# Kernel tuning notes

Hardware: AMD Instinct MI355X
Metric: run time of the kernel (lower is better)

Reference implementation:

```python
import jax, jax.numpy as jnp
import numpy as np

B = 65536   # batch
F = 256     # FeatureDim
E = 8       # experts_num
D = 64      # ExpertOutDim
EPS = 1e-5  # BatchNorm eps (eval mode: running stats)


def _bn(x, g, be, m, v):
    # BatchNorm1d in eval mode
    return (x - m) * jax.lax.rsqrt(v + EPS) * g + be


def setup_inputs() -> dict:
    key = jax.random.key(0)
    ks = jax.random.split(key, 40)
    r = lambda i, s: jax.random.normal(ks[i], s, dtype=jnp.float32) * 0.05
    u = lambda i, s: jax.random.uniform(ks[i], s, dtype=jnp.float32)
    return dict(
        signal_em=jax.random.normal(ks[0], (B, F), dtype=jnp.float32),
        muti_em=jax.random.normal(ks[1], (B, F), dtype=jnp.float32),
        similarity=jax.random.uniform(ks[2], (B,), dtype=jnp.float32),
        w=u(3, ()), b=u(4, ()),
        ps_W=r(5, (F, 256)), ps_b=r(6, (256,)), ps_g=u(7, (256,)), ps_be=r(8, (256,)), ps_m=r(9, (256,)), ps_v=u(10, (256,)) + 0.5,
        pm_W=r(11, (F, 256)), pm_b=r(12, (256,)), pm_g=u(13, (256,)), pm_be=r(14, (256,)), pm_m=r(15, (256,)), pm_v=u(16, (256,)) + 0.5,
        c1_W=r(17, (2 * F, 64)), c1_b=r(18, (64,)), c1_g=u(19, (64,)), c1_be=r(20, (64,)), c1_m=r(21, (64,)), c1_v=u(22, (64,)) + 0.5,
        c2_W=r(23, (64, 64)), c2_b=r(24, (64,)), c2_g=u(25, (64,)), c2_be=r(26, (64,)), c2_m=r(27, (64,)), c2_v=u(28, (64,)) + 0.5,
        c3_W=r(29, (64, 2)), c3_b=r(30, (2,)),
        e_W1=r(31, (E, 2 * F, 256)), e_b1=r(32, (E, 256)),
        e_W2=r(33, (E, 256, D)), e_b2=r(34, (E, D)),
        s_W1=r(35, (E, E)), s_b1=r(36, (E,)), s_W2=r(37, (E, E)), s_b2=r(38, (E,)),
    )


def reference(signal_em, muti_em, similarity, w, b,
              ps_W, ps_b, ps_g, ps_be, ps_m, ps_v,
              pm_W, pm_b, pm_g, pm_be, pm_m, pm_v,
              c1_W, c1_b, c1_g, c1_be, c1_m, c1_v,
              c2_W, c2_b, c2_g, c2_be, c2_m, c2_v,
              c3_W, c3_b,
              e_W1, e_b1, e_W2, e_b2,
              s_W1, s_b1, s_W2, s_b2):
    sim_weight = similarity[:, None] * w + b                        # [B,1]
    sig = jax.nn.relu(_bn(signal_em @ ps_W + ps_b, ps_g, ps_be, ps_m, ps_v))
    sig = sim_weight * sig
    mut = jax.nn.relu(_bn(muti_em @ pm_W + pm_b, pm_g, pm_be, pm_m, pm_v))
    temp = jnp.concatenate([sig, mut], axis=1)                      # [B, 512]

    # classifier head (dropout = identity in eval mode)
    h = jax.nn.relu(_bn(temp @ c1_W + c1_b, c1_g, c1_be, c1_m, c1_v))
    h = jax.nn.relu(_bn(h @ c2_W + c2_b, c2_g, c2_be, c2_m, c2_v))
    pre_score = h @ c3_W + c3_b                                     # [B,2]

    # all E experts as one batched GEMM (Expert_net has dropout p=0)
    eh = jax.nn.relu(jnp.einsum('bf,efh->beh', temp, e_W1) + e_b1)  # [B,E,256]
    eo = jax.nn.relu(jnp.einsum('beh,ehd->bed', eh, e_W2) + e_b2)   # [B,E,64]

    # SE-style gating: avg/max pool over expert-out dim (kernel==D -> scalar)
    att_ave = eo.mean(axis=-1)                                      # [B,E]
    att_max = eo.max(axis=-1)                                       # [B,E]
    senet = lambda x: jax.nn.gelu(x @ s_W1 + s_b1, approximate=False) @ s_W2 + s_b2
    wts = jax.nn.sigmoid(senet(att_ave) + senet(att_max))           # [B,E]

    gate_out = jnp.einsum('bed,be->bd', eo, wts)                    # [B,D]
    return (gate_out, pre_score)
```

## Files before the change

### kernel.cpp

```cpp
#include <hip/hip_runtime.h>
#include <math.h>

using u32 = unsigned int;
using u16 = unsigned short;
typedef __attribute__((ext_vector_type(4))) float f4;
typedef __attribute__((ext_vector_type(4))) u32 u4;
typedef __attribute__((ext_vector_type(2))) u32 u2;
typedef __attribute__((ext_vector_type(8))) __bf16 b8;

union U4B8 { u4 u; b8 b; };

__device__ __forceinline__ u16 f2b(float x) {
  u32 u = __float_as_uint(x);
  u32 r = (u + 0x7FFFu + ((u >> 16) & 1u)) >> 16;
  return (u16)r;
}
__device__ __forceinline__ u32 pack2(float a, float b) { return (u32)f2b(a) | ((u32)f2b(b) << 16); }
__device__ __forceinline__ f4 mfma16(b8 a, b8 b, f4 c) {
  return __builtin_amdgcn_mfma_f32_16x16x32_bf16(a, b, c, 0, 0, 0);
}

#define FENCE() asm volatile("" ::: "memory")
#define RAWBAR() do { FENCE(); __builtin_amdgcn_s_barrier(); FENCE(); __builtin_amdgcn_sched_barrier(0); } while (0)
#define VMW(nlit) do { asm volatile("s_waitcnt vmcnt(" nlit ")" ::: "memory"); __builtin_amdgcn_sched_barrier(0); } while (0)
#define LGKM0() do { asm volatile("s_waitcnt lgkmcnt(0)" ::: "memory"); __builtin_amdgcn_sched_barrier(0); } while (0)
#define LBAR() do { LGKM0(); __builtin_amdgcn_s_barrier(); FENCE(); __builtin_amdgcn_sched_barrier(0); } while (0)

template <int NB>
__device__ __forceinline__ void gstage(const u16* g, u16* l, int t) {
#pragma unroll
  for (int i = 0; i < NB; i += 8192) {
    __builtin_amdgcn_global_load_lds(
        (__attribute__((address_space(1))) u32*)(g + (i >> 1) + t * 8),
        (__attribute__((address_space(3))) u32*)(l + (i >> 1) + ((t >> 6) << 9)),
        16, 0, 0);
  }
}

__global__ void prep_kernel(
    const float* __restrict__ ps_W, const float* __restrict__ ps_b, const float* __restrict__ ps_g,
    const float* __restrict__ ps_be, const float* __restrict__ ps_m, const float* __restrict__ ps_v,
    const float* __restrict__ pm_W, const float* __restrict__ pm_b, const float* __restrict__ pm_g,
    const float* __restrict__ pm_be, const float* __restrict__ pm_m, const float* __restrict__ pm_v,
    const float* __restrict__ c1_W, const float* __restrict__ c1_b, const float* __restrict__ c1_g,
    const float* __restrict__ c1_be, const float* __restrict__ c1_m, const float* __restrict__ c1_v,
    const float* __restrict__ c2_W, const float* __restrict__ c2_b, const float* __restrict__ c2_g,
    const float* __restrict__ c2_be, const float* __restrict__ c2_m, const float* __restrict__ c2_v,
    u16* __restrict__ pst, u16* __restrict__ pmt,
    u16* __restrict__ c1t, u16* __restrict__ c2t, float* __restrict__ fold)
{
  int i0 = blockIdx.x * blockDim.x + threadIdx.x;
  int stride = gridDim.x * blockDim.x;
  for (int idx = i0; idx < 65536; idx += stride) {
    int s = idx >> 14; int rem = idx & 16383;
    int n = rem >> 6, q = rem & 63;
    int k = s * 64 + (q ^ ((n & 7) << 3));
    pst[idx] = f2b(ps_W[k * 256 + n]);
    pmt[idx] = f2b(pm_W[k * 256 + n]);
  }
  for (int idx = i0; idx < 64 * 512; idx += stride) {
    int n = idx >> 9, q = idx & 511;
    int k = q ^ ((n & 7) << 3);
    c1t[idx] = f2b(c1_W[k * 64 + n]);
  }
  for (int idx = i0; idx < 64 * 64; idx += stride) {
    int n = idx >> 6, k = idx & 63;
    c2t[idx] = f2b(c2_W[k * 64 + n]);
  }
  for (int idx = i0; idx < 256; idx += stride) {
    float a = ps_g[idx] * rsqrtf(ps_v[idx] + 1e-5f);
    fold[idx] = a; fold[256 + idx] = (ps_b[idx] - ps_m[idx]) * a + ps_be[idx];
    float a2 = pm_g[idx] * rsqrtf(pm_v[idx] + 1e-5f);
    fold[512 + idx] = a2; fold[768 + idx] = (pm_b[idx] - pm_m[idx]) * a2 + pm_be[idx];
  }
  for (int idx = i0; idx < 64; idx += stride) {
    float a = c1_g[idx] * rsqrtf(c1_v[idx] + 1e-5f);
    fold[1024 + idx] = a; fold[1088 + idx] = (c1_b[idx] - c1_m[idx]) * a + c1_be[idx];
    float a2 = c2_g[idx] * rsqrtf(c2_v[idx] + 1e-5f);
    fold[1152 + idx] = a2; fold[1216 + idx] = (c2_b[idx] - c2_m[idx]) * a2 + c2_be[idx];
  }
}

__global__ __launch_bounds__(512, 4) void k1_kernel(
    const float* __restrict__ sig, const float* __restrict__ mut,
    const float* __restrict__ simil, const float* __restrict__ wS, const float* __restrict__ bS,
    const u16* __restrict__ pst, const u16* __restrict__ pmt,
    const float* __restrict__ fold, u16* __restrict__ temp,
    const float* __restrict__ e_W1, const float* __restrict__ e_W2,
    u16* __restrict__ w1t, u16* __restrict__ w2t)
{
  extern __shared__ __align__(16) u16 smk[];
  const int t = threadIdx.x;
  if (blockIdx.y == 2) {
    int i0 = blockIdx.x * 512 + t;
    const int stride = 1024 * 512;
    for (int idx = i0; idx < 8 * 256 * 512; idx += stride) {
      int e = idx >> 17; int rem = idx & 131071;
      int S = rem >> 13; int rem2 = rem & 8191;
      int nl = rem2 >> 6; int q = rem2 & 63;
      int n = (S & 1) * 128 + nl;
      int k = (S >> 1) * 64 + (q ^ ((nl & 7) << 3));
      w1t[idx] = f2b(e_W1[e * 131072 + k * 256 + n]);
    }
    for (int idx = i0; idx < 8 * 64 * 256; idx += stride) {
      int e = idx >> 14; int rem = idx & 16383;
      int d = rem >> 8; int q = rem & 255;
      int h = q ^ ((d & 7) << 3);
      w2t[idx] = f2b(e_W2[e * 16384 + h * 64 + d]);
    }
    return;
  }
  const int w = t >> 6, l = t & 63;
  const int lr = l & 15, lk = (l >> 4) * 8, lv = (l >> 4) * 4;
  const int xoru = (l & 7) << 3;
  const int rg = w >> 1, cg = w & 1;
  const int half = blockIdx.y;
  const float* X = half ? mut : sig;
  const u16* Wt = half ? pmt : pst;
  const int rb = blockIdx.x;
  const int rg0 = rb * 64;
  const f4 ZF = {0.f, 0.f, 0.f, 0.f};
  const int myrow = rg * 16 + lr;

  f4 xr[16];
  {
    const float* xp = X + (rg0 + myrow) * 256 + lk;
#pragma unroll
    for (int c = 0; c < 8; ++c) {
      xr[2 * c]     = *(const f4*)(xp + c * 32);
      xr[2 * c + 1] = *(const f4*)(xp + c * 32 + 4);
    }
  }
  float swv = 1.f;
  if (half == 0) swv = simil[rg0 + myrow] * wS[0] + bS[0];
  gstage<32768>(Wt, smk, t);
  b8 af[8];
#pragma unroll
  for (int c = 0; c < 8; ++c) {
    U4B8 tmp;
    tmp.u[0] = pack2(xr[2 * c][0], xr[2 * c][1]);
    tmp.u[1] = pack2(xr[2 * c][2], xr[2 * c][3]);
    tmp.u[2] = pack2(xr[2 * c + 1][0], xr[2 * c + 1][1]);
    tmp.u[3] = pack2(xr[2 * c + 1][2], xr[2 * c + 1][3]);
    af[c] = tmp.b;
  }

  f4 acc[8];
#pragma unroll
  for (int i = 0; i < 8; ++i) acc[i] = ZF;

#define K1P(P, STG) do { \
    VMW("0"); RAWBAR(); \
    STG; \
    __builtin_amdgcn_s_setprio(1); \
    _Pragma("unroll") for (int kk = 0; kk < 2; ++kk) { \
      b8 bf[8]; \
      _Pragma("unroll") for (int nf = 0; nf < 8; ++nf) \
        bf[nf] = *(const b8*)(smk + ((P) & 1) * 16384 + (cg * 128 + nf * 16 + lr) * 64 + ((kk * 32 + lk) ^ xoru)); \
      _Pragma("unroll") for (int nf = 0; nf < 8; ++nf) \
        acc[nf] = mfma16(bf[nf], af[(P) * 2 + kk], acc[nf]); \
    } \
    __builtin_amdgcn_s_setprio(0); \
  } while (0)

  K1P(0, gstage<32768>(Wt + 16384, smk + 16384, t));
  K1P(1, gstage<32768>(Wt + 32768, smk, t));
  K1P(2, gstage<32768>(Wt + 49152, smk + 16384, t));
  K1P(3, (void)0);
#undef K1P

#pragma unroll
  for (int nf = 0; nf < 8; ++nf) {
    int col = cg * 128 + nf * 16 + lv;
    const f4 al = *(const f4*)(fold + half * 512 + col);
    const f4 be = *(const f4*)(fold + half * 512 + 256 + col);
    float v0 = fmaxf(acc[nf][0] * al[0] + be[0], 0.f) * swv;
    float v1 = fmaxf(acc[nf][1] * al[1] + be[1], 0.f) * swv;
    float v2 = fmaxf(acc[nf][2] * al[2] + be[2], 0.f) * swv;
    float v3 = fmaxf(acc[nf][3] * al[3] + be[3], 0.f) * swv;
    u2 pv; pv[0] = pack2(v0, v1); pv[1] = pack2(v2, v3);
    int st = col >> 6;
    int kin = col & 63;
    int q = kin ^ ((myrow & 7) << 3);
    *(u2*)(smk + st * 4096 + myrow * 64 + q) = pv;
  }
  LBAR();
  {
    u16* dst = temp + (rb >> 1) * 65536 + half * 32768 + (rb & 1) * 4096;
#pragma unroll
    for (int st = 0; st < 4; ++st) {
      u4 v = *(const u4*)(smk + st * 4096 + t * 8);
      *(u4*)(dst + st * 8192 + t * 8) = v;
    }
  }
}

__global__ __launch_bounds__(512, 2) void k2_kernel(
    u16* __restrict__ temp, const u16* __restrict__ w1t, const u16* __restrict__ w2t,
    const u16* __restrict__ c1t, const u16* __restrict__ c2t,
    const float* __restrict__ fold,
    const float* __restrict__ c3W, const float* __restrict__ c3B,
    const float* __restrict__ eb1, const float* __restrict__ eb2,
    const float* __restrict__ sW1, const float* __restrict__ sB1,
    const float* __restrict__ sW2, const float* __restrict__ sB2,
    float* __restrict__ outp)
{
  extern __shared__ __align__(16) u16 sm[];
  u16* smW  = sm;
  u16* smE  = sm + 32768;
  u16* smR2 = sm + 49152;
  float* attA  = (float*)(sm + 65536);
  float* attM  = attA + 1024;
  float* wtsb  = attM + 1024;
  float* c3sm  = wtsb + 1024;
  float* eb1sm = c3sm + 136;
  float* eb2sm = eb1sm + 2048;

  const int t = threadIdx.x, w = t >> 6, l = t & 63;
  const int lr = l & 15, lk = (l >> 4) * 8, lv = (l >> 4) * 4;
  const int xoru = (l & 7) << 3;
  const int rg = w >> 1, cg = w & 1;
  const int rg0 = blockIdx.x * 128;
  const f4 ZF = {0.f, 0.f, 0.f, 0.f};
  u16* tempE = temp + blockIdx.x * 65536;

  b8 af[16][2];

#define AFLOAD(R) { \
    _Pragma("unroll") for (int c8 = 0; c8 < 8; ++c8) { \
      _Pragma("unroll") for (int mi = 0; mi < 2; ++mi) \
        af[(R) * 8 + c8][mi] = *(const b8*)(smE + (c8 >> 1) * 8192 + (rg * 32 + mi * 16 + lr) * 64 + ((((c8 & 1) * 32) + lk) ^ xoru)); \
    } }

  {
    for (int z = t; z < 2048; z += 512) attA[z] = 0.f;
    f4 rEb1 = *(const f4*)(eb1 + t * 4);
    f4 rEb2 = ZF; if (t < 128) rEb2 = *(const f4*)(eb2 + t * 4);
    float rC3 = 0.f; if (t < 128) rC3 = c3W[t]; else if (t < 130) rC3 = c3B[t - 128];
    u4 rC2 = *(const u4*)(c2t + (t >> 3) * 64 + (t & 7) * 8);

    gstage<65536>(tempE, smE, t);
    gstage<65536>(c1t, smW, t);
    *(f4*)(eb1sm + t * 4) = rEb1;
    if (t < 128) *(f4*)(eb2sm + t * 4) = rEb2;
    if (t < 130) c3sm[t] = rC3;
    VMW("8"); RAWBAR();
    AFLOAD(0);
    asm volatile("s_waitcnt lgkmcnt(0)" ::: "memory");
    RAWBAR();
    gstage<65536>(tempE + 32768, smE, t);
    VMW("8"); RAWBAR();
    f4 ah[2][2] = {{ZF, ZF}, {ZF, ZF}};
#define HPART(R) { \
    __builtin_amdgcn_s_setprio(1); \
    _Pragma("unroll") for (int c8 = 0; c8 < 8; ++c8) { \
      _Pragma("unroll") for (int nf = 0; nf < 2; ++nf) { \
        b8 ch = *(const b8*)(smW + (cg * 32 + nf * 16 + lr) * 512 + ((((R) * 8 + c8) * 32 + lk) ^ xoru)); \
        _Pragma("unroll") for (int mi = 0; mi < 2; ++mi) \
          ah[nf][mi] = mfma16(ch, af[(R) * 8 + c8][mi], ah[nf][mi]); \
      } } \
    __builtin_amdgcn_s_setprio(0); }
    HPART(0)
    VMW("0"); RAWBAR();
    AFLOAD(1);
    HPART(1)
#undef HPART
    asm volatile("s_waitcnt lgkmcnt(0)" ::: "memory");
    RAWBAR();
    u16* h1b = smE;
    u16* c2sm = smR2;
    u16* h2b = smR2 + 4608;
#pragma unroll
    for (int nf = 0; nf < 2; ++nf) {
      int col = cg * 32 + nf * 16 + lv;
      const f4 av1 = *(const f4*)(fold + 1024 + col);
      const f4 bv1 = *(const f4*)(fold + 1088 + col);
#pragma unroll
      for (int mi = 0; mi < 2; ++mi) {
        int row = rg * 32 + mi * 16 + lr;
        u2 pv;
        pv[0] = pack2(fmaxf(ah[nf][mi][0] * av1[0] + bv1[0], 0.f), fmaxf(ah[nf][mi][1] * av1[1] + bv1[1], 0.f));
        pv[1] = pack2(fmaxf(ah[nf][mi][2] * av1[2] + bv1[2], 0.f), fmaxf(ah[nf][mi][3] * av1[3] + bv1[3], 0.f));
        *(u2*)(h1b + row * 72 + col) = pv;
      }
    }
    *(u4*)(c2sm + (t >> 3) * 72 + (t & 7) * 8) = rC2;
    LBAR();
    f4 a2[2][2] = {{ZF, ZF}, {ZF, ZF}};
#pragma unroll
    for (int kk = 0; kk < 2; ++kk) {
      b8 hf[2], cf[2];
#pragma unroll
      for (int mi = 0; mi < 2; ++mi)
        hf[mi] = *(const b8*)(h1b + (rg * 32 + mi * 16 + lr) * 72 + kk * 32 + lk);
#pragma unroll
      for (int nf = 0; nf < 2; ++nf)
        cf[nf] = *(const b8*)(c2sm + (cg * 32 + nf * 16 + lr) * 72 + kk * 32 + lk);
#pragma unroll
      for (int mi = 0; mi < 2; ++mi)
#pragma unroll
        for (int nf = 0; nf < 2; ++nf)
          a2[mi][nf] = mfma16(cf[nf], hf[mi], a2[mi][nf]);
    }
#pragma unroll
    for (int nf = 0; nf < 2; ++nf) {
      int col = cg * 32 + nf * 16 + lv;
      const f4 av2 = *(const f4*)(fold + 1152 + col);
      const f4 bv2 = *(const f4*)(fold + 1216 + col);
#pragma unroll
      for (int mi = 0; mi < 2; ++mi) {
        int row = rg * 32 + mi * 16 + lr;
        u2 pv;
        pv[0] = pack2(fmaxf(a2[mi][nf][0] * av2[0] + bv2[0], 0.f), fmaxf(a2[mi][nf][1] * av2[1] + bv2[1], 0.f));
        pv[1] = pack2(fmaxf(a2[mi][nf][2] * av2[2] + bv2[2], 0.f), fmaxf(a2[mi][nf][3] * av2[3] + bv2[3], 0.f));
        *(u2*)(h2b + row * 72 + col) = pv;
      }
    }
    LBAR();
    if (t < 256) {
      int row = t >> 1, c = t & 1;
      float s_ = c3sm[128 + c];
#pragma unroll
      for (int j = 0; j < 8; ++j) {
        u4 hv = *(const u4*)(h2b + row * 72 + j * 8);
#pragma unroll
        for (int q = 0; q < 4; ++q) {
          float lo = __uint_as_float(hv[q] << 16);
          float hi = __uint_as_float(hv[q] & 0xffff0000u);
          s_ += lo * c3sm[(j * 8 + q * 2) * 2 + c];
          s_ += hi * c3sm[(j * 8 + q * 2 + 1) * 2 + c];
        }
      }
      outp[4194304 + (rg0 + row) * 2 + c] = s_;
    }
    RAWBAR();
    gstage<32768>(w1t, smW, t);
  }

#define SUB(S, NW, STG) do { \
    VMW(NW); RAWBAR(); \
    STG; \
    __builtin_amdgcn_s_setprio(1); \
    _Pragma("unroll") for (int kk = 0; kk < 2; ++kk) { \
      b8 bf[4]; \
      _Pragma("unroll") for (int nf = 0; nf < 4; ++nf) \
        bf[nf] = *(const b8*)(smW + ((S) & 3) * 8192 + (cg * 64 + nf * 16 + lr) * 64 + ((kk * 32 + lk) ^ xoru)); \
      _Pragma("unroll") for (int nf = 0; nf < 4; ++nf) \
        _Pragma("unroll") for (int mi = 0; mi < 2; ++mi) \
          acc[((S) & 1) * 4 + nf][mi] = mfma16(bf[nf], af[((S) >> 1) * 2 + kk][mi], acc[((S) & 1) * 4 + nf][mi]); \
    } \
    __builtin_amdgcn_s_setprio(0); \
  } while (0)

#define G16(SRC, DST) gstage<16384>((SRC), (DST), t)

#define EHEPI(E, H, DST) { \
    _Pragma("unroll") for (int nf = 0; nf < 4; ++nf) { \
      int colL = cg * 64 + nf * 16 + lv; \
      const f4 bv = *(const f4*)(eb1sm + (E) * 256 + (H) * 128 + colL); \
      _Pragma("unroll") for (int mi = 0; mi < 2; ++mi) { \
        int row = rg * 32 + mi * 16 + lr; \
        f4 a_ = acc[(H) * 4 + nf][mi]; \
        u2 pv; \
        pv[0] = pack2(fmaxf(a_[0] + bv[0], 0.f), fmaxf(a_[1] + bv[1], 0.f)); \
        pv[1] = pack2(fmaxf(a_[2] + bv[2], 0.f), fmaxf(a_[3] + bv[3], 0.f)); \
        *(u2*)((DST) + row * 128 + (colL ^ xoru)) = pv; \
      } } }

#define G2ALL() do { \
    __builtin_amdgcn_s_setprio(1); \
    _Pragma("unroll") for (int kq = 0; kq < 8; ++kq) { \
      const u16* ebase = (kq < 4) ? smE : (smW + 16384); \
      b8 wf[2], ef[2]; \
      _Pragma("unroll") for (int nf = 0; nf < 2; ++nf) \
        wf[nf] = *(const b8*)(smR2 + (cg * 32 + nf * 16 + lr) * 256 + ((kq * 32 + lk) ^ xoru)); \
      _Pragma("unroll") for (int mi = 0; mi < 2; ++mi) \
        ef[mi] = *(const b8*)(ebase + (rg * 32 + mi * 16 + lr) * 128 + ((((kq & 3) * 32) + lk) ^ xoru)); \
      _Pragma("unroll") for (int mi = 0; mi < 2; ++mi) \
        _Pragma("unroll") for (int nf = 0; nf < 2; ++nf) \
          e2[mi][nf] = mfma16(wf[nf], ef[mi], e2[mi][nf]); \
    } \
    __builtin_amdgcn_s_setprio(0); \
  } while (0)

#define POOLX(EE) do { \
    _Pragma("unroll") for (int mi = 0; mi < 2; ++mi) { \
      int row = rg * 32 + mi * 16 + lr; \
      float s_ = 0.f, mx = 0.f; \
      _Pragma("unroll") for (int nf = 0; nf < 2; ++nf) { \
        int d0 = cg * 32 + nf * 16 + lv; \
        const f4 bv2 = *(const f4*)(eb2sm + (EE) * 64 + d0); \
        float v0 = fmaxf(e2[mi][nf][0] + bv2[0], 0.f); \
        float v1 = fmaxf(e2[mi][nf][1] + bv2[1], 0.f); \
        float v2 = fmaxf(e2[mi][nf][2] + bv2[2], 0.f); \
        float v3 = fmaxf(e2[mi][nf][3] + bv2[3], 0.f); \
        s_ += v0 + v1 + v2 + v3; \
        mx = fmaxf(mx, fmaxf(fmaxf(v0, v1), fmaxf(v2, v3))); \
        u2 pv; pv[0] = pack2(v0, v1); pv[1] = pack2(v2, v3); \
        *(u2*)(tempE + (EE) * 8192 + row * 64 + d0) = pv; \
      } \
      s_ += __shfl_xor(s_, 16); s_ += __shfl_xor(s_, 32); \
      mx = fmaxf(mx, __shfl_xor(mx, 16)); mx = fmaxf(mx, __shfl_xor(mx, 32)); \
      if (l < 16) { \
        atomicAdd(attA + row * 8 + (EE), s_); \
        atomicMax((unsigned int*)(attM + row * 8 + (EE)), __float_as_uint(mx)); \
      } \
    } \
  } while (0)

#define EXPERT(E, NW0, NW1, NW15, NWPOST) { \
    const u16* w1E = w1t + (E) * 131072; \
    f4 acc[8][2]; \
    _Pragma("unroll") for (int nf = 0; nf < 8; ++nf) \
      _Pragma("unroll") for (int mi = 0; mi < 2; ++mi) acc[nf][mi] = ZF; \
    SUB(0, NW0, G16(w1E + 2 * 8192, smW + 2 * 8192)); \
    SUB(1, NW1, G16(w1E + 3 * 8192, smW + 3 * 8192)); \
    SUB(2, "2", G16(w1E + 4 * 8192, smW + 0 * 8192)); \
    SUB(3, "2", G16(w1E + 5 * 8192, smW + 1 * 8192)); \
    SUB(4, "2", G16(w1E + 6 * 8192, smW + 2 * 8192)); \
    SUB(5, "2", G16(w1E + 7 * 8192, smW + 3 * 8192)); \
    SUB(6, "2", G16(w1E + 8 * 8192, smW + 0 * 8192)); \
    SUB(7, "2", G16(w1E + 9 * 8192, smW + 1 * 8192)); \
    SUB(8, "2", G16(w1E + 10 * 8192, smW + 2 * 8192)); \
    SUB(9, "2", G16(w1E + 11 * 8192, smW + 3 * 8192)); \
    SUB(10, "2", G16(w1E + 12 * 8192, smW + 0 * 8192)); \
    SUB(11, "2", G16(w1E + 13 * 8192, smW + 1 * 8192)); \
    SUB(12, "2", G16(w1E + 14 * 8192, smW + 2 * 8192)); \
    SUB(13, "2", { G16(w1E + 15 * 8192, smW + 3 * 8192); \
                   gstage<32768>(w2t + (E) * 16384, smR2, t); }); \
    SUB(14, "6", { if ((E) < 7) G16(w1t + ((E) + 1) * 131072, smW); }); \
    SUB(15, NW15, { if ((E) < 7) G16(w1t + ((E) + 1) * 131072 + 8192, smW + 8192); }); \
    EHEPI(E, 0, smE) \
    RAWBAR();  \
    EHEPI(E, 1, smW + 16384) \
    VMW(NWPOST); LBAR();  \
    f4 e2[2][2]; \
    e2[0][0] = ZF; e2[0][1] = ZF; e2[1][0] = ZF; e2[1][1] = ZF; \
    G2ALL(); \
    POOLX(E); \
  }

  EXPERT(0, "2", "2", "6", "4")
  EXPERT(1, "6", "6", "6", "4")
  EXPERT(2, "6", "6", "6", "4")
  EXPERT(3, "6", "6", "6", "4")
  EXPERT(4, "6", "6", "6", "4")
  EXPERT(5, "6", "6", "6", "4")
  EXPERT(6, "6", "6", "6", "4")
  EXPERT(7, "6", "6", "4", "0")
#undef EXPERT
#undef SUB
#undef G16
#undef EHEPI
#undef G2ALL

  VMW("0");
  LBAR();
  if (t < 128) {
    float xa[8], xm[8], ga[8], gm[8];
#pragma unroll
    for (int j = 0; j < 8; ++j) {
      xa[j] = attA[t * 8 + j] * 0.015625f;
      xm[j] = attM[t * 8 + j];
    }
#pragma unroll
    for (int j = 0; j < 8; ++j) {
      float a1 = sB1[j], a2 = sB1[j];
#pragma unroll
      for (int i = 0; i < 8; ++i) { float wv = sW1[i * 8 + j]; a1 += xa[i] * wv; a2 += xm[i] * wv; }
      ga[j] = 0.5f * a1 * (1.f + erff(a1 * 0.70710678118654752f));
      gm[j] = 0.5f * a2 * (1.f + erff(a2 * 0.70710678118654752f));
    }
#pragma unroll
    for (int j = 0; j < 8; ++j) {
      float o1 = sB2[j], o2 = sB2[j];
#pragma unroll
      for (int i = 0; i < 8; ++i) { float wv = sW2[i * 8 + j]; o1 += ga[i] * wv; o2 += gm[i] * wv; }
      float z = o1 + o2;
      wtsb[t * 8 + j] = 1.f / (1.f + expf(-z));
    }
  }
  LBAR();
  {
    int grow = t >> 2, gd0 = (t & 3) * 16;
    float wv[8];
#pragma unroll
    for (int e2_ = 0; e2_ < 8; ++e2_) wv[e2_] = wtsb[grow * 8 + e2_];
    float g[16];
#pragma unroll
    for (int j = 0; j < 16; ++j) g[j] = 0.f;
#pragma unroll
    for (int e2_ = 0; e2_ < 8; ++e2_) {
      const u16* wsE = tempE + e2_ * 8192 + grow * 64 + gd0;
      u4 qa = *(const u4*)(wsE); u4 qb = *(const u4*)(wsE + 8);
#pragma unroll
      for (int q = 0; q < 4; ++q) {
        g[2 * q + 0] += wv[e2_] * __uint_as_float(qa[q] << 16);
        g[2 * q + 1] += wv[e2_] * __uint_as_float(qa[q] & 0xffff0000u);
        g[8 + 2 * q + 0] += wv[e2_] * __uint_as_float(qb[q] << 16);
        g[8 + 2 * q + 1] += wv[e2_] * __uint_as_float(qb[q] & 0xffff0000u);
      }
    }
    float* op = outp + (rg0 + grow) * 64 + gd0;
    f4 o0 = {g[0], g[1], g[2], g[3]}, o1 = {g[4], g[5], g[6], g[7]};
    f4 o2 = {g[8], g[9], g[10], g[11]}, o3 = {g[12], g[13], g[14], g[15]};
    *(f4*)op = o0; *(f4*)(op + 4) = o1; *(f4*)(op + 8) = o2; *(f4*)(op + 12) = o3;
  }
}

extern "C" void kernel_launch(void* const* d_in, const int* in_sizes, int n_in,
                              void* d_out, int out_size, void* d_ws, size_t ws_size,
                              hipStream_t stream) {
  const float* signal = (const float*)d_in[0];
  const float* muti   = (const float*)d_in[1];
  const float* simil  = (const float*)d_in[2];
  const float* wS     = (const float*)d_in[3];
  const float* bS     = (const float*)d_in[4];
  const float* ps_W = (const float*)d_in[5];  const float* ps_b = (const float*)d_in[6];
  const float* ps_g = (const float*)d_in[7];  const float* ps_be = (const float*)d_in[8];
  const float* ps_m = (const float*)d_in[9];  const float* ps_v = (const float*)d_in[10];
  const float* pm_W = (const float*)d_in[11]; const float* pm_b = (const float*)d_in[12];
  const float* pm_g = (const float*)d_in[13]; const float* pm_be = (const float*)d_in[14];
  const float* pm_m = (const float*)d_in[15]; const float* pm_v = (const float*)d_in[16];
  const float* c1_W = (const float*)d_in[17]; const float* c1_b = (const float*)d_in[18];
  const float* c1_g = (const float*)d_in[19]; const float* c1_be = (const float*)d_in[20];
  const float* c1_m = (const float*)d_in[21]; const float* c1_v = (const float*)d_in[22];
  const float* c2_W = (const float*)d_in[23]; const float* c2_b = (const float*)d_in[24];
  const float* c2_g = (const float*)d_in[25]; const float* c2_be = (const float*)d_in[26];
  const float* c2_m = (const float*)d_in[27]; const float* c2_v = (const float*)d_in[28];
  const float* c3_W = (const float*)d_in[29]; const float* c3_b = (const float*)d_in[30];
  const float* e_W1 = (const float*)d_in[31]; const float* e_b1 = (const float*)d_in[32];
  const float* e_W2 = (const float*)d_in[33]; const float* e_b2 = (const float*)d_in[34];
  const float* s_W1 = (const float*)d_in[35]; const float* s_b1 = (const float*)d_in[36];
  const float* s_W2 = (const float*)d_in[37]; const float* s_b2 = (const float*)d_in[38];

  char* ws = (char*)d_ws;
  u16* temp = (u16*)ws;
  u16* w1t  = (u16*)(ws + 67108864);
  u16* w2t  = (u16*)(ws + 69206016);
  u16* pst  = (u16*)(ws + 69468160);
  u16* pmt  = (u16*)(ws + 69599232);
  u16* c1t  = (u16*)(ws + 69730304);
  u16* c2t  = (u16*)(ws + 69795840);
  float* fold = (float*)(ws + 69804032);
  float* outp = (float*)d_out;

  prep_kernel<<<dim3(256), dim3(256), 0, stream>>>(
      ps_W, ps_b, ps_g, ps_be, ps_m, ps_v, pm_W, pm_b, pm_g, pm_be, pm_m, pm_v,
      c1_W, c1_b, c1_g, c1_be, c1_m, c1_v, c2_W, c2_b, c2_g, c2_be, c2_m, c2_v,
      pst, pmt, c1t, c2t, fold);
  k1_kernel<<<dim3(1024, 3), dim3(512), 65536, stream>>>(
      signal, muti, simil, wS, bS, pst, pmt, fold, temp, e_W1, e_W2, w1t, w2t);
  k2_kernel<<<dim3(512), dim3(512), 154144, stream>>>(
      temp, w1t, w2t, c1t, c2t, fold, c3_W, c3_b, e_b1, e_b2, s_W1, s_b1, s_W2, s_b2, outp);
}
```

Measured before the change: 262.0 us.

## Prefetch next sub-tile's first-half B fragments across the barrier in expert GEMM

Restructures the expert W1 pipeline so each sub-step reads the first k-half of the next slot's B fragments from LDS into registers before waiting on the barrier. The wait and barrier move to the end of each step, and the prologue stages three slots ahead instead of two. The aim is to hide LDS read latency behind the barrier and deepen global prefetch. In exchange it uses more registers, re-tunes the vmcnt waits, and carries a risk of LDS hazards if the waits are miscounted.

```diff
diff --git a/kernel.cpp b/kernel.cpp
--- a/kernel.cpp
+++ b/kernel.cpp
@@ -225,12 +225,18 @@
   u16* tempE = temp + blockIdx.x * 65536;
 
   b8 af[16][2];
+  b8 preA[4];
 
 #define AFLOAD(R) { \
     _Pragma("unroll") for (int c8 = 0; c8 < 8; ++c8) { \
       _Pragma("unroll") for (int mi = 0; mi < 2; ++mi) \
         af[(R) * 8 + c8][mi] = *(const b8*)(smE + (c8 >> 1) * 8192 + (rg * 32 + mi * 16 + lr) * 64 + ((((c8 & 1) * 32) + lk) ^ xoru)); \
     } }
+
+#define PRERD(SL) { \
+    _Pragma("unroll") for (int nf = 0; nf < 4; ++nf) \
+      preA[nf] = *(const b8*)(smW + (SL) * 8192 + (cg * 64 + nf * 16 + lr) * 64 + (lk ^ xoru)); \
+  }
 
   {
     for (int z = t; z < 2048; z += 512) attA[z] = 0.f;
@@ -334,22 +340,27 @@
       outp[4194304 + (rg0 + row) * 2 + c] = s_;
     }
     RAWBAR();
-    gstage<32768>(w1t, smW, t);
-  }
-
-#define SUB(S, NW, STG) do { \
-    VMW(NW); RAWBAR(); \
-    STG; \
+    gstage<49152>(w1t, smW, t);
+    VMW("0"); RAWBAR();
+    PRERD(0)
+  }
+
+#define SUBX(S, NW, PT, PEND, DOPEND, ...) do { \
+    if (PT) { PRERD((S) & 3) } \
+    __VA_ARGS__; \
     __builtin_amdgcn_s_setprio(1); \
-    _Pragma("unroll") for (int kk = 0; kk < 2; ++kk) { \
-      b8 bf[4]; \
+    _Pragma("unroll") for (int nf = 0; nf < 4; ++nf) \
+      _Pragma("unroll") for (int mi = 0; mi < 2; ++mi) \
+        acc[((S) & 1) * 4 + nf][mi] = mfma16(preA[nf], af[((S) >> 1) * 2][mi], acc[((S) & 1) * 4 + nf][mi]); \
+    { b8 bf1[4]; \
       _Pragma("unroll") for (int nf = 0; nf < 4; ++nf) \
-        bf[nf] = *(const b8*)(smW + ((S) & 3) * 8192 + (cg * 64 + nf * 16 + lr) * 64 + ((kk * 32 + lk) ^ xoru)); \
+        bf1[nf] = *(const b8*)(smW + ((S) & 3) * 8192 + (cg * 64 + nf * 16 + lr) * 64 + ((32 + lk) ^ xoru)); \
       _Pragma("unroll") for (int nf = 0; nf < 4; ++nf) \
         _Pragma("unroll") for (int mi = 0; mi < 2; ++mi) \
-          acc[((S) & 1) * 4 + nf][mi] = mfma16(bf[nf], af[((S) >> 1) * 2 + kk][mi], acc[((S) & 1) * 4 + nf][mi]); \
-    } \
+          acc[((S) & 1) * 4 + nf][mi] = mfma16(bf1[nf], af[((S) >> 1) * 2 + 1][mi], acc[((S) & 1) * 4 + nf][mi]); } \
     __builtin_amdgcn_s_setprio(0); \
+    if (DOPEND) { PRERD(PEND) } \
+    VMW(NW); RAWBAR(); \
   } while (0)
 
 #define G16(SRC, DST) gstage<16384>((SRC), (DST), t)
@@ -408,48 +419,49 @@
     } \
   } while (0)
 
-#define EXPERT(E, NW0, NW1, NW15, NWPOST) { \
+#define EXPERT(E, NW0, NW13, NW14, DP15) { \
     const u16* w1E = w1t + (E) * 131072; \
     f4 acc[8][2]; \
     _Pragma("unroll") for (int nf = 0; nf < 8; ++nf) \
       _Pragma("unroll") for (int mi = 0; mi < 2; ++mi) acc[nf][mi] = ZF; \
-    SUB(0, NW0, G16(w1E + 2 * 8192, smW + 2 * 8192)); \
-    SUB(1, NW1, G16(w1E + 3 * 8192, smW + 3 * 8192)); \
-    SUB(2, "2", G16(w1E + 4 * 8192, smW + 0 * 8192)); \
-    SUB(3, "2", G16(w1E + 5 * 8192, smW + 1 * 8192)); \
-    SUB(4, "2", G16(w1E + 6 * 8192, smW + 2 * 8192)); \
-    SUB(5, "2", G16(w1E + 7 * 8192, smW + 3 * 8192)); \
-    SUB(6, "2", G16(w1E + 8 * 8192, smW + 0 * 8192)); \
-    SUB(7, "2", G16(w1E + 9 * 8192, smW + 1 * 8192)); \
-    SUB(8, "2", G16(w1E + 10 * 8192, smW + 2 * 8192)); \
-    SUB(9, "2", G16(w1E + 11 * 8192, smW + 3 * 8192)); \
-    SUB(10, "2", G16(w1E + 12 * 8192, smW + 0 * 8192)); \
-    SUB(11, "2", G16(w1E + 13 * 8192, smW + 1 * 8192)); \
-    SUB(12, "2", G16(w1E + 14 * 8192, smW + 2 * 8192)); \
-    SUB(13, "2", { G16(w1E + 15 * 8192, smW + 3 * 8192); \
-                   gstage<32768>(w2t + (E) * 16384, smR2, t); }); \
-    SUB(14, "6", { if ((E) < 7) G16(w1t + ((E) + 1) * 131072, smW); }); \
-    SUB(15, NW15, { if ((E) < 7) G16(w1t + ((E) + 1) * 131072 + 8192, smW + 8192); }); \
+    SUBX(0, NW0, 0, 1, 1, { G16(w1E + 3 * 8192, smW + 3 * 8192); \
+                            if ((E) != 0) G16(w1E + 2 * 8192, smW + 2 * 8192); }); \
+    SUBX(1, "2", 0, 0, 0, G16(w1E + 4 * 8192, smW + 0 * 8192)); \
+    SUBX(2, "2", 1, 3, 1, G16(w1E + 5 * 8192, smW + 1 * 8192)); \
+    SUBX(3, "2", 0, 0, 1, G16(w1E + 6 * 8192, smW + 2 * 8192)); \
+    SUBX(4, "2", 0, 1, 1, G16(w1E + 7 * 8192, smW + 3 * 8192)); \
+    SUBX(5, "2", 0, 2, 1, G16(w1E + 8 * 8192, smW + 0 * 8192)); \
+    SUBX(6, "2", 0, 3, 1, G16(w1E + 9 * 8192, smW + 1 * 8192)); \
+    SUBX(7, "2", 0, 0, 1, G16(w1E + 10 * 8192, smW + 2 * 8192)); \
+    SUBX(8, "2", 0, 1, 1, G16(w1E + 11 * 8192, smW + 3 * 8192)); \
+    SUBX(9, "2", 0, 2, 1, G16(w1E + 12 * 8192, smW + 0 * 8192)); \
+    SUBX(10, "2", 0, 3, 1, G16(w1E + 13 * 8192, smW + 1 * 8192)); \
+    SUBX(11, "2", 0, 0, 1, G16(w1E + 14 * 8192, smW + 2 * 8192)); \
+    SUBX(12, "6", 0, 1, 1, { G16(w1E + 15 * 8192, smW + 3 * 8192); \
+                             gstage<32768>(w2t + (E) * 16384, smR2, t); }); \
+    SUBX(13, NW13, 0, 2, 1, { if ((E) < 7) G16(w1t + ((E) + 1) * 131072, smW + 0 * 8192); }); \
+    SUBX(14, NW14, 0, 3, 1, { if ((E) < 7) G16(w1t + ((E) + 1) * 131072 + 8192, smW + 1 * 8192); }); \
+    SUBX(15, "0", 0, 0, DP15, (void)0); \
     EHEPI(E, 0, smE) \
-    RAWBAR();  \
     EHEPI(E, 1, smW + 16384) \
-    VMW(NWPOST); LBAR();  \
+    LBAR();  \
     f4 e2[2][2]; \
     e2[0][0] = ZF; e2[0][1] = ZF; e2[1][0] = ZF; e2[1][1] = ZF; \
     G2ALL(); \
     POOLX(E); \
-  }
-
-  EXPERT(0, "2", "2", "6", "4")
-  EXPERT(1, "6", "6", "6", "4")
-  EXPERT(2, "6", "6", "6", "4")
-  EXPERT(3, "6", "6", "6", "4")
-  EXPERT(4, "6", "6", "6", "4")
-  EXPERT(5, "6", "6", "6", "4")
-  EXPERT(6, "6", "6", "6", "4")
-  EXPERT(7, "6", "6", "4", "0")
+    RAWBAR();  \
+  }
+
+  EXPERT(0, "2", "6", "2", 1)
+  EXPERT(1, "4", "6", "2", 1)
+  EXPERT(2, "4", "6", "2", 1)
+  EXPERT(3, "4", "6", "2", 1)
+  EXPERT(4, "4", "6", "2", 1)
+  EXPERT(5, "4", "6", "2", 1)
+  EXPERT(6, "4", "6", "2", 1)
+  EXPERT(7, "4", "4", "0", 0)
 #undef EXPERT
-#undef SUB
+#undef SUBX
 #undef G16
 #undef EHEPI
 #undef G2ALL
```

Measured after the change: 260.3 us, median of 3. No clear change (-0.7%).

## Halve k2 block to 256 threads with 64-row warp tiles and N-outer expert loop

Applied to the files above, without the earlier changes.

The main k2 kernel now runs with 256 threads instead of 512. Each warp computes 64 rows (4 M-fragments) instead of 32, which raises register-level reuse of each loaded B fragment. The expert W1 weights are re-laid out so the N half is the outer dimension, letting the accumulator shrink to 4x4 fragments and the first-half epilogue run mid-expert. Staging loops, wait counts and the final gating loop are rescaled to match. The sched_barrier hints in the sync macros are removed. In exchange, each block has fewer waves to hide latency and per-thread register pressure rises.

```diff
diff --git a/kernel.cpp b/kernel.cpp
--- a/kernel.cpp
+++ b/kernel.cpp
@@ -21,15 +21,15 @@
 }
 
 #define FENCE() asm volatile("" ::: "memory")
-#define RAWBAR() do { FENCE(); __builtin_amdgcn_s_barrier(); FENCE(); __builtin_amdgcn_sched_barrier(0); } while (0)
-#define VMW(nlit) do { asm volatile("s_waitcnt vmcnt(" nlit ")" ::: "memory"); __builtin_amdgcn_sched_barrier(0); } while (0)
-#define LGKM0() do { asm volatile("s_waitcnt lgkmcnt(0)" ::: "memory"); __builtin_amdgcn_sched_barrier(0); } while (0)
-#define LBAR() do { LGKM0(); __builtin_amdgcn_s_barrier(); FENCE(); __builtin_amdgcn_sched_barrier(0); } while (0)
-
-template <int NB>
+#define RAWBAR() do { FENCE(); __builtin_amdgcn_s_barrier(); FENCE(); } while (0)
+#define VMW(nlit) asm volatile("s_waitcnt vmcnt(" nlit ")" ::: "memory")
+#define LGKM0() asm volatile("s_waitcnt lgkmcnt(0)" ::: "memory")
+#define LBAR() do { LGKM0(); FENCE(); __builtin_amdgcn_s_barrier(); FENCE(); } while (0)
+
+template <int NB, int STEP>
 __device__ __forceinline__ void gstage(const u16* g, u16* l, int t) {
 #pragma unroll
-  for (int i = 0; i < NB; i += 8192) {
+  for (int i = 0; i < NB; i += STEP) {
     __builtin_amdgcn_global_load_lds(
         (__attribute__((address_space(1))) u32*)(g + (i >> 1) + t * 8),
         (__attribute__((address_space(3))) u32*)(l + (i >> 1) + ((t >> 6) << 9)),
@@ -98,8 +98,8 @@
       int e = idx >> 17; int rem = idx & 131071;
       int S = rem >> 13; int rem2 = rem & 8191;
       int nl = rem2 >> 6; int q = rem2 & 63;
-      int n = (S & 1) * 128 + nl;
-      int k = (S >> 1) * 64 + (q ^ ((nl & 7) << 3));
+      int n = (S >> 3) * 128 + nl;
+      int k = (S & 7) * 64 + (q ^ ((nl & 7) << 3));
       w1t[idx] = f2b(e_W1[e * 131072 + k * 256 + n]);
     }
     for (int idx = i0; idx < 8 * 64 * 256; idx += stride) {
@@ -133,7 +133,7 @@
   }
   float swv = 1.f;
   if (half == 0) swv = simil[rg0 + myrow] * wS[0] + bS[0];
-  gstage<32768>(Wt, smk, t);
+  gstage<32768, 8192>(Wt, smk, t);
   b8 af[8];
 #pragma unroll
   for (int c = 0; c < 8; ++c) {
@@ -149,9 +149,9 @@
 #pragma unroll
   for (int i = 0; i < 8; ++i) acc[i] = ZF;
 
-#define K1P(P, STG) do { \
+#define K1P(P, ...) do { \
     VMW("0"); RAWBAR(); \
-    STG; \
+    __VA_ARGS__; \
     __builtin_amdgcn_s_setprio(1); \
     _Pragma("unroll") for (int kk = 0; kk < 2; ++kk) { \
       b8 bf[8]; \
@@ -163,9 +163,9 @@
     __builtin_amdgcn_s_setprio(0); \
   } while (0)
 
-  K1P(0, gstage<32768>(Wt + 16384, smk + 16384, t));
-  K1P(1, gstage<32768>(Wt + 32768, smk, t));
-  K1P(2, gstage<32768>(Wt + 49152, smk + 16384, t));
+  K1P(0, (gstage<32768, 8192>(Wt + 16384, smk + 16384, t)));
+  K1P(1, (gstage<32768, 8192>(Wt + 32768, smk, t)));
+  K1P(2, (gstage<32768, 8192>(Wt + 49152, smk + 16384, t)));
   K1P(3, (void)0);
 #undef K1P
 
@@ -195,7 +195,7 @@
   }
 }
 
-__global__ __launch_bounds__(512, 2) void k2_kernel(
+__global__ __launch_bounds__(256, 1) void k2_kernel(
     u16* __restrict__ temp, const u16* __restrict__ w1t, const u16* __restrict__ w2t,
     const u16* __restrict__ c1t, const u16* __restrict__ c2t,
     const float* __restrict__ fold,
@@ -224,39 +224,46 @@
   const f4 ZF = {0.f, 0.f, 0.f, 0.f};
   u16* tempE = temp + blockIdx.x * 65536;
 
-  b8 af[16][2];
+  b8 af[16][4];
 
 #define AFLOAD(R) { \
     _Pragma("unroll") for (int c8 = 0; c8 < 8; ++c8) { \
-      _Pragma("unroll") for (int mi = 0; mi < 2; ++mi) \
-        af[(R) * 8 + c8][mi] = *(const b8*)(smE + (c8 >> 1) * 8192 + (rg * 32 + mi * 16 + lr) * 64 + ((((c8 & 1) * 32) + lk) ^ xoru)); \
+      _Pragma("unroll") for (int mi = 0; mi < 4; ++mi) \
+        af[(R) * 8 + c8][mi] = *(const b8*)(smE + (c8 >> 1) * 8192 + (rg * 64 + mi * 16 + lr) * 64 + ((((c8 & 1) * 32) + lk) ^ xoru)); \
     } }
 
   {
-    for (int z = t; z < 2048; z += 512) attA[z] = 0.f;
-    f4 rEb1 = *(const f4*)(eb1 + t * 4);
+    for (int z = t; z < 2048; z += 256) attA[z] = 0.f;
+    f4 rEb1a = *(const f4*)(eb1 + t * 4);
+    f4 rEb1b = *(const f4*)(eb1 + 1024 + t * 4);
     f4 rEb2 = ZF; if (t < 128) rEb2 = *(const f4*)(eb2 + t * 4);
     float rC3 = 0.f; if (t < 128) rC3 = c3W[t]; else if (t < 130) rC3 = c3B[t - 128];
-    u4 rC2 = *(const u4*)(c2t + (t >> 3) * 64 + (t & 7) * 8);
-
-    gstage<65536>(tempE, smE, t);
-    gstage<65536>(c1t, smW, t);
-    *(f4*)(eb1sm + t * 4) = rEb1;
+    u4 rC2a = *(const u4*)(c2t + (t >> 3) * 64 + (t & 7) * 8);
+    u4 rC2b = *(const u4*)(c2t + ((t + 256) >> 3) * 64 + ((t + 256) & 7) * 8);
+
+    gstage<65536, 4096>(tempE, smE, t);
+    gstage<65536, 4096>(c1t, smW, t);
+    *(f4*)(eb1sm + t * 4) = rEb1a;
+    *(f4*)(eb1sm + 1024 + t * 4) = rEb1b;
     if (t < 128) *(f4*)(eb2sm + t * 4) = rEb2;
     if (t < 130) c3sm[t] = rC3;
-    VMW("8"); RAWBAR();
+    VMW("16"); RAWBAR();
     AFLOAD(0);
-    asm volatile("s_waitcnt lgkmcnt(0)" ::: "memory");
+    LGKM0();
     RAWBAR();
-    gstage<65536>(tempE + 32768, smE, t);
-    VMW("8"); RAWBAR();
-    f4 ah[2][2] = {{ZF, ZF}, {ZF, ZF}};
+    gstage<65536, 4096>(tempE + 32768, smE, t);
+    VMW("16"); RAWBAR();
+    f4 ah[2][4];
+#pragma unroll
+    for (int nf = 0; nf < 2; ++nf)
+#pragma unroll
+      for (int mi = 0; mi < 4; ++mi) ah[nf][mi] = ZF;
 #define HPART(R) { \
     __builtin_amdgcn_s_setprio(1); \
     _Pragma("unroll") for (int c8 = 0; c8 < 8; ++c8) { \
       _Pragma("unroll") for (int nf = 0; nf < 2; ++nf) { \
         b8 ch = *(const b8*)(smW + (cg * 32 + nf * 16 + lr) * 512 + ((((R) * 8 + c8) * 32 + lk) ^ xoru)); \
-        _Pragma("unroll") for (int mi = 0; mi < 2; ++mi) \
+        _Pragma("unroll") for (int mi = 0; mi < 4; ++mi) \
           ah[nf][mi] = mfma16(ch, af[(R) * 8 + c8][mi], ah[nf][mi]); \
       } } \
     __builtin_amdgcn_s_setprio(0); }
@@ -265,7 +272,7 @@
     AFLOAD(1);
     HPART(1)
 #undef HPART
-    asm volatile("s_waitcnt lgkmcnt(0)" ::: "memory");
+    LGKM0();
     RAWBAR();
     u16* h1b = smE;
     u16* c2sm = smR2;
@@ -276,28 +283,33 @@
       const f4 av1 = *(const f4*)(fold + 1024 + col);
       const f4 bv1 = *(const f4*)(fold + 1088 + col);
 #pragma unroll
-      for (int mi = 0; mi < 2; ++mi) {
-        int row = rg * 32 + mi * 16 + lr;
+      for (int mi = 0; mi < 4; ++mi) {
+        int row = rg * 64 + mi * 16 + lr;
         u2 pv;
         pv[0] = pack2(fmaxf(ah[nf][mi][0] * av1[0] + bv1[0], 0.f), fmaxf(ah[nf][mi][1] * av1[1] + bv1[1], 0.f));
         pv[1] = pack2(fmaxf(ah[nf][mi][2] * av1[2] + bv1[2], 0.f), fmaxf(ah[nf][mi][3] * av1[3] + bv1[3], 0.f));
         *(u2*)(h1b + row * 72 + col) = pv;
       }
     }
-    *(u4*)(c2sm + (t >> 3) * 72 + (t & 7) * 8) = rC2;
+    *(u4*)(c2sm + (t >> 3) * 72 + (t & 7) * 8) = rC2a;
+    *(u4*)(c2sm + ((t + 256) >> 3) * 72 + ((t + 256) & 7) * 8) = rC2b;
     LBAR();
-    f4 a2[2][2] = {{ZF, ZF}, {ZF, ZF}};
+    f4 a2[4][2];
+#pragma unroll
+    for (int mi = 0; mi < 4; ++mi)
+#pragma unroll
+      for (int nf = 0; nf < 2; ++nf) a2[mi][nf] = ZF;
 #pragma unroll
     for (int kk = 0; kk < 2; ++kk) {
-      b8 hf[2], cf[2];
-#pragma unroll
-      for (int mi = 0; mi < 2; ++mi)
-        hf[mi] = *(const b8*)(h1b + (rg * 32 + mi * 16 + lr) * 72 + kk * 32 + lk);
+      b8 hf[4], cf[2];
+#pragma unroll
+      for (int mi = 0; mi < 4; ++mi)
+        hf[mi] = *(const b8*)(h1b + (rg * 64 + mi * 16 + lr) * 72 + kk * 32 + lk);
 #pragma unroll
       for (int nf = 0; nf < 2; ++nf)
         cf[nf] = *(const b8*)(c2sm + (cg * 32 + nf * 16 + lr) * 72 + kk * 32 + lk);
 #pragma unroll
-      for (int mi = 0; mi < 2; ++mi)
+      for (int mi = 0; mi < 4; ++mi)
 #pragma unroll
         for (int nf = 0; nf < 2; ++nf)
           a2[mi][nf] = mfma16(cf[nf], hf[mi], a2[mi][nf]);
@@ -308,8 +320,8 @@
       const f4 av2 = *(const f4*)(fold + 1152 + col);
       const f4 bv2 = *(const f4*)(fold + 1216 + col);
 #pragma unroll
-      for (int mi = 0; mi < 2; ++mi) {
-        int row = rg * 32 + mi * 16 + lr;
+      for (int mi = 0; mi < 4; ++mi) {
+        int row = rg * 64 + mi * 16 + lr;
         u2 pv;
         pv[0] = pack2(fmaxf(a2[mi][nf][0] * av2[0] + bv2[0], 0.f), fmaxf(a2[mi][nf][1] * av2[1] + bv2[1], 0.f));
         pv[1] = pack2(fmaxf(a2[mi][nf][2] * av2[2] + bv2[2], 0.f), fmaxf(a2[mi][nf][3] * av2[3] + bv2[3], 0.f));
@@ -317,7 +329,7 @@
       }
     }
     LBAR();
-    if (t < 256) {
+    {
       int row = t >> 1, c = t & 1;
       float s_ = c3sm[128 + c];
 #pragma unroll
@@ -334,49 +346,54 @@
       outp[4194304 + (rg0 + row) * 2 + c] = s_;
     }
     RAWBAR();
-    gstage<32768>(w1t, smW, t);
-  }
-
-#define SUB(S, NW, STG) do { \
+    gstage<16384, 4096>(w1t, smW, t);
+    gstage<16384, 4096>(w1t + 8192, smW + 8192, t);
+  }
+
+#define SUB(S, NW, ...) do { \
     VMW(NW); RAWBAR(); \
-    STG; \
+    __VA_ARGS__; \
     __builtin_amdgcn_s_setprio(1); \
     _Pragma("unroll") for (int kk = 0; kk < 2; ++kk) { \
       b8 bf[4]; \
       _Pragma("unroll") for (int nf = 0; nf < 4; ++nf) \
         bf[nf] = *(const b8*)(smW + ((S) & 3) * 8192 + (cg * 64 + nf * 16 + lr) * 64 + ((kk * 32 + lk) ^ xoru)); \
       _Pragma("unroll") for (int nf = 0; nf < 4; ++nf) \
-        _Pragma("unroll") for (int mi = 0; mi < 2; ++mi) \
-          acc[((S) & 1) * 4 + nf][mi] = mfma16(bf[nf], af[((S) >> 1) * 2 + kk][mi], acc[((S) & 1) * 4 + nf][mi]); \
+        _Pragma("unroll") for (int mi = 0; mi < 4; ++mi) \
+          acc[nf][mi] = mfma16(bf[nf], af[((S) & 7) * 2 + kk][mi], acc[nf][mi]); \
     } \
     __builtin_amdgcn_s_setprio(0); \
   } while (0)
 
-#define G16(SRC, DST) gstage<16384>((SRC), (DST), t)
+#define G16(SRC, DST) gstage<16384, 4096>((SRC), (DST), t)
 
 #define EHEPI(E, H, DST) { \
     _Pragma("unroll") for (int nf = 0; nf < 4; ++nf) { \
       int colL = cg * 64 + nf * 16 + lv; \
       const f4 bv = *(const f4*)(eb1sm + (E) * 256 + (H) * 128 + colL); \
-      _Pragma("unroll") for (int mi = 0; mi < 2; ++mi) { \
-        int row = rg * 32 + mi * 16 + lr; \
-        f4 a_ = acc[(H) * 4 + nf][mi]; \
+      _Pragma("unroll") for (int mi = 0; mi < 4; ++mi) { \
+        int row = rg * 64 + mi * 16 + lr; \
+        f4 a_ = acc[nf][mi]; \
         u2 pv; \
         pv[0] = pack2(fmaxf(a_[0] + bv[0], 0.f), fmaxf(a_[1] + bv[1], 0.f)); \
         pv[1] = pack2(fmaxf(a_[2] + bv[2], 0.f), fmaxf(a_[3] + bv[3], 0.f)); \
         *(u2*)((DST) + row * 128 + (colL ^ xoru)) = pv; \
       } } }
 
+#define ACCZERO() { \
+    _Pragma("unroll") for (int nf = 0; nf < 4; ++nf) \
+      _Pragma("unroll") for (int mi = 0; mi < 4; ++mi) acc[nf][mi] = ZF; }
+
 #define G2ALL() do { \
     __builtin_amdgcn_s_setprio(1); \
     _Pragma("unroll") for (int kq = 0; kq < 8; ++kq) { \
       const u16* ebase = (kq < 4) ? smE : (smW + 16384); \
-      b8 wf[2], ef[2]; \
+      b8 wf[2], ef[4]; \
       _Pragma("unroll") for (int nf = 0; nf < 2; ++nf) \
         wf[nf] = *(const b8*)(smR2 + (cg * 32 + nf * 16 + lr) * 256 + ((kq * 32 + lk) ^ xoru)); \
-      _Pragma("unroll") for (int mi = 0; mi < 2; ++mi) \
-        ef[mi] = *(const b8*)(ebase + (rg * 32 + mi * 16 + lr) * 128 + ((((kq & 3) * 32) + lk) ^ xoru)); \
-      _Pragma("unroll") for (int mi = 0; mi < 2; ++mi) \
+      _Pragma("unroll") for (int mi = 0; mi < 4; ++mi) \
+        ef[mi] = *(const b8*)(ebase + (rg * 64 + mi * 16 + lr) * 128 + ((((kq & 3) * 32) + lk) ^ xoru)); \
+      _Pragma("unroll") for (int mi = 0; mi < 4; ++mi) \
         _Pragma("unroll") for (int nf = 0; nf < 2; ++nf) \
           e2[mi][nf] = mfma16(wf[nf], ef[mi], e2[mi][nf]); \
     } \
@@ -384,8 +401,8 @@
   } while (0)
 
 #define POOLX(EE) do { \
-    _Pragma("unroll") for (int mi = 0; mi < 2; ++mi) { \
-      int row = rg * 32 + mi * 16 + lr; \
+    _Pragma("unroll") for (int mi = 0; mi < 4; ++mi) { \
+      int row = rg * 64 + mi * 16 + lr; \
       float s_ = 0.f, mx = 0.f; \
       _Pragma("unroll") for (int nf = 0; nf < 2; ++nf) { \
         int d0 = cg * 32 + nf * 16 + lv; \
@@ -410,48 +427,50 @@
 
 #define EXPERT(E, NW0, NW1, NW15, NWPOST) { \
     const u16* w1E = w1t + (E) * 131072; \
-    f4 acc[8][2]; \
-    _Pragma("unroll") for (int nf = 0; nf < 8; ++nf) \
-      _Pragma("unroll") for (int mi = 0; mi < 2; ++mi) acc[nf][mi] = ZF; \
+    f4 acc[4][4]; \
+    ACCZERO() \
     SUB(0, NW0, G16(w1E + 2 * 8192, smW + 2 * 8192)); \
     SUB(1, NW1, G16(w1E + 3 * 8192, smW + 3 * 8192)); \
-    SUB(2, "2", G16(w1E + 4 * 8192, smW + 0 * 8192)); \
-    SUB(3, "2", G16(w1E + 5 * 8192, smW + 1 * 8192)); \
-    SUB(4, "2", G16(w1E + 6 * 8192, smW + 2 * 8192)); \
-    SUB(5, "2", G16(w1E + 7 * 8192, smW + 3 * 8192)); \
-    SUB(6, "2", G16(w1E + 8 * 8192, smW + 0 * 8192)); \
-    SUB(7, "2", G16(w1E + 9 * 8192, smW + 1 * 8192)); \
-    SUB(8, "2", G16(w1E + 10 * 8192, smW + 2 * 8192)); \
-    SUB(9, "2", G16(w1E + 11 * 8192, smW + 3 * 8192)); \
-    SUB(10, "2", G16(w1E + 12 * 8192, smW + 0 * 8192)); \
-    SUB(11, "2", G16(w1E + 13 * 8192, smW + 1 * 8192)); \
-    SUB(12, "2", G16(w1E + 14 * 8192, smW + 2 * 8192)); \
-    SUB(13, "2", { G16(w1E + 15 * 8192, smW + 3 * 8192); \
-                   gstage<32768>(w2t + (E) * 16384, smR2, t); }); \
-    SUB(14, "6", { if ((E) < 7) G16(w1t + ((E) + 1) * 131072, smW); }); \
+    SUB(2, "4", G16(w1E + 4 * 8192, smW + 0 * 8192)); \
+    SUB(3, "4", G16(w1E + 5 * 8192, smW + 1 * 8192)); \
+    SUB(4, "4", G16(w1E + 6 * 8192, smW + 2 * 8192)); \
+    SUB(5, "4", G16(w1E + 7 * 8192, smW + 3 * 8192)); \
+    SUB(6, "4", G16(w1E + 8 * 8192, smW + 0 * 8192)); \
+    SUB(7, "4", G16(w1E + 9 * 8192, smW + 1 * 8192)); \
+    EHEPI(E, 0, smE)    \
+    ACCZERO() \
+    SUB(8, "4", G16(w1E + 10 * 8192, smW + 2 * 8192)); \
+    SUB(9, "4", G16(w1E + 11 * 8192, smW + 3 * 8192)); \
+    SUB(10, "4", G16(w1E + 12 * 8192, smW + 0 * 8192)); \
+    SUB(11, "4", G16(w1E + 13 * 8192, smW + 1 * 8192)); \
+    SUB(12, "4", G16(w1E + 14 * 8192, smW + 2 * 8192)); \
+    SUB(13, "4", { G16(w1E + 15 * 8192, smW + 3 * 8192); \
+                   gstage<32768, 4096>(w2t + (E) * 16384, smR2, t); }); \
+    SUB(14, "12", { if ((E) < 7) G16(w1t + ((E) + 1) * 131072, smW); }); \
     SUB(15, NW15, { if ((E) < 7) G16(w1t + ((E) + 1) * 131072 + 8192, smW + 8192); }); \
-    EHEPI(E, 0, smE) \
     RAWBAR();  \
     EHEPI(E, 1, smW + 16384) \
     VMW(NWPOST); LBAR();  \
-    f4 e2[2][2]; \
-    e2[0][0] = ZF; e2[0][1] = ZF; e2[1][0] = ZF; e2[1][1] = ZF; \
+    f4 e2[4][2]; \
+    _Pragma("unroll") for (int mi = 0; mi < 4; ++mi) \
+      _Pragma("unroll") for (int nf = 0; nf < 2; ++nf) e2[mi][nf] = ZF; \
     G2ALL(); \
     POOLX(E); \
   }
 
-  EXPERT(0, "2", "2", "6", "4")
-  EXPERT(1, "6", "6", "6", "4")
-  EXPERT(2, "6", "6", "6", "4")
-  EXPERT(3, "6", "6", "6", "4")
-  EXPERT(4, "6", "6", "6", "4")
-  EXPERT(5, "6", "6", "6", "4")
-  EXPERT(6, "6", "6", "6", "4")
-  EXPERT(7, "6", "6", "4", "0")
+  EXPERT(0, "4",  "4",  "12", "8")
+  EXPERT(1, "12", "12", "12", "8")
+  EXPERT(2, "12", "12", "12", "8")
+  EXPERT(3, "12", "12", "12", "8")
+  EXPERT(4, "12", "12", "12", "8")
+  EXPERT(5, "12", "12", "12", "8")
+  EXPERT(6, "12", "12", "12", "8")
+  EXPERT(7, "12", "12", "8",  "0")
 #undef EXPERT
 #undef SUB
 #undef G16
 #undef EHEPI
+#undef ACCZERO
 #undef G2ALL
 
   VMW("0");
@@ -481,8 +500,9 @@
     }
   }
   LBAR();
-  {
-    int grow = t >> 2, gd0 = (t & 3) * 16;
+  for (int hh = 0; hh < 2; ++hh) {
+    int tt = t + hh * 256;
+    int grow = tt >> 2, gd0 = (tt & 3) * 16;
     float wv[8];
 #pragma unroll
     for (int e2_ = 0; e2_ < 8; ++e2_) wv[e2_] = wtsb[grow * 8 + e2_];
@@ -551,6 +571,6 @@
       pst, pmt, c1t, c2t, fold);
   k1_kernel<<<dim3(1024, 3), dim3(512), 65536, stream>>>(
       signal, muti, simil, wS, bS, pst, pmt, fold, temp, e_W1, e_W2, w1t, w2t);
-  k2_kernel<<<dim3(512), dim3(512), 154144, stream>>>(
+  k2_kernel<<<dim3(512), dim3(256), 154144, stream>>>(
       temp, w1t, w2t, c1t, c2t, fold, c3_W, c3_b, e_b1, e_b2, s_W1, s_b1, s_W2, s_b2, outp);
 }
```

Measured after the change: 311.5 us. 18.9% more time.
